# Kernel tuning notes

Measured on AMD Instinct MI355X. Metric: run time of the kernel, lower is better.

Reference implementation:

```python
import jax, jax.numpy as jnp
import numpy as np

N = 4608      # total nodes (48 graphs x 96 nodes)
B = 48
NPG = 96
D = 512       # vec_dim
XD = 16       # x_dim
E = N * 32    # GAT edges
L = 6         # GAT layers


def _w(k, shape, fan_in):
    return jax.random.normal(k, shape, jnp.float32) * (1.0 / np.sqrt(fan_in))


def setup_inputs() -> dict:
    key = jax.random.key(0)
    ks = jax.random.split(key, 24)
    x = jax.random.normal(ks[0], (N, XD), jnp.float32)
    xyz = jax.random.normal(ks[1], (N, 3), jnp.float32)
    edge_index = jax.random.randint(ks[2], (2, E), 0, N, dtype=jnp.int32)
    ptr = (jnp.arange(B + 1) * NPG).astype(jnp.int32)
    # complete graph with replacement per segment (torch.combinations order: i<=j)
    i, j = np.triu_indices(NPG)
    offs = (np.arange(B) * NPG)[:, None]
    cloud_edge_index = jnp.asarray(
        np.stack([(i[None, :] + offs).reshape(-1), (j[None, :] + offs).reshape(-1)]),
        jnp.int32)
    return {
        'x': x, 'edge_index': edge_index, 'ptr': ptr, 'xyz': xyz,
        'cloud_edge_index': cloud_edge_index,
        'x_proj_w': _w(ks[3], (XD, D), XD), 'x_proj_b': jnp.zeros((D,), jnp.float32),
        'gat_wl': _w(ks[4], (L, D, D), D), 'gat_bl': jnp.zeros((L, D), jnp.float32),
        'gat_wr': _w(ks[5], (L, D, D), D), 'gat_br': jnp.zeros((L, D), jnp.float32),
        'gat_att': _w(ks[6], (L, D), D), 'gat_bias': jnp.zeros((L, D), jnp.float32),
        'gat_ln_g': jnp.ones((L - 1, D), jnp.float32), 'gat_ln_b': jnp.zeros((L - 1, D), jnp.float32),
        'cg_xyz_w': _w(ks[7], (3, D), 3),
        'cg_bn_g': jnp.ones((D,), jnp.float32), 'cg_bn_b': jnp.zeros((D,), jnp.float32),
        'cg_lin1_w': _w(ks[8], (D, D), D), 'cg_lin1_b': jnp.zeros((D,), jnp.float32),
        'cg_ln_g': jnp.ones((D,), jnp.float32), 'cg_ln_b': jnp.zeros((D,), jnp.float32),
        'lin_w': _w(ks[9], (D, D), D), 'lin_b': jnp.zeros((D,), jnp.float32),
        'bn_g': jnp.ones((D,), jnp.float32), 'bn_b': jnp.zeros((D,), jnp.float32),
    }


def _batchnorm(t, g, b):
    mu = t.mean(0)
    v = ((t - mu) ** 2).mean(0)
    return (t - mu) / jnp.sqrt(v + 1e-5) * g + b


def _forward(x, edge_index, cloud_edge_index, x_proj_w, x_proj_b, gat_wl, gat_bl,
             gat_wr, gat_br, gat_att, gat_bias, gat_ln_g, gat_ln_b, cg_xyz_w,
             cg_bn_g, cg_bn_b, cg_lin1_w, cg_lin1_b, cg_ln_g, cg_ln_b,
             lin_w, lin_b, bn_g, bn_b, xyz):
    n = x.shape[0]
    h = x @ x_proj_w + x_proj_b  # [N, D]
    # ---- GATv2 stack (heads=1, self-loops added, eval mode: no dropout) ----
    loops = jnp.arange(n, dtype=edge_index.dtype)
    ei = jnp.concatenate([edge_index, jnp.stack([loops, loops])], axis=1)
    src, dst = ei[0], ei[1]
    xg = h
    for l in range(L):
        xl = xg @ gat_wl[l] + gat_bl[l]
        xr = xg @ gat_wr[l] + gat_br[l]
        e = jax.nn.leaky_relu(xl[src] + xr[dst], 0.2) @ gat_att[l]  # [E+N]
        m = jax.ops.segment_max(e, dst, num_segments=n)
        ew = jnp.exp(e - m[dst])
        den = jax.ops.segment_sum(ew, dst, num_segments=n)
        alpha = ew / den[dst]
        out = jax.ops.segment_sum(alpha[:, None] * xl[src], dst, num_segments=n) + gat_bias[l]
        if l < L - 1:
            # PyG LayerNorm, mode='graph', batch=None: normalize over all elements
            mu = out.mean()
            sd = jnp.sqrt(((out - mu) ** 2).mean())
            out = (out - mu) / (sd + 1e-5) * gat_ln_g[l] + gat_ln_b[l]
            out = jax.nn.relu(out)
        xg = out
    # ---- CloudGraph (complete graph gather-compute-scatter) ----
    a, b = cloud_edge_index[0], cloud_edge_index[1]
    rx = h[a] - h[b]          # [Ec, D]
    rz = xyz[a] - xyz[b]      # [Ec, 3]
    sq = (rz ** 2).sum(-1)
    dist = jnp.where(sq > 0, jnp.sqrt(jnp.where(sq > 0, sq, 1.0)), 0.0)
    w = jnp.exp(-dist)[:, None]
    p1 = jax.ops.segment_sum(jax.nn.relu((w * rx) @ cg_lin1_w + cg_lin1_b), a, num_segments=n)
    mu1 = p1.mean(-1, keepdims=True)
    v1 = ((p1 - mu1) ** 2).mean(-1, keepdims=True)
    ln1 = (p1 - mu1) / jnp.sqrt(v1 + 1e-5) * cg_ln_g + cg_ln_b
    p2 = jax.ops.segment_sum(jax.nn.relu(rz @ cg_xyz_w), a, num_segments=n)
    xc = h + ln1 + _batchnorm(p2, cg_bn_g, cg_bn_b)
    # ---- fuse + final norm ----
    return _batchnorm((h + xg + xc) @ lin_w + lin_b, bn_g, bn_b)


def reference(x, edge_index, ptr, xyz, cloud_edge_index, x_proj_w, x_proj_b,
              gat_wl, gat_bl, gat_wr, gat_br, gat_att, gat_bias, gat_ln_g,
              gat_ln_b, cg_xyz_w, cg_bn_g, cg_bn_b, cg_lin1_w, cg_lin1_b,
              cg_ln_g, cg_ln_b, lin_w, lin_b, bn_g, bn_b):
    return _forward(x, edge_index, cloud_edge_index, x_proj_w, x_proj_b, gat_wl,
                    gat_bl, gat_wr, gat_br, gat_att, gat_bias, gat_ln_g,
                    gat_ln_b, cg_xyz_w, cg_bn_g, cg_bn_b, cg_lin1_w, cg_lin1_b,
                    cg_ln_g, cg_ln_b, lin_w, lin_b, bn_g, bn_b, xyz)
```

## Files before the change

### kernel.cpp

```cpp
#include <hip/hip_runtime.h>
#include <hip/hip_bf16.h>

#define NN 4608
#define BG 48
#define NPG 96
#define DD 512
#define XDIM 16
#define EREAL 147456
#define NLAYER 6
#define NK 262144
#define TRIU 4656

typedef __hip_bfloat16 bf16;
typedef short short8 __attribute__((ext_vector_type(8)));
typedef float f32x4 __attribute__((ext_vector_type(4)));
typedef float f32x2 __attribute__((ext_vector_type(2)));

__device__ __forceinline__ float s2f(short s) {
  return __uint_as_float(((unsigned int)(unsigned short)s) << 16);
}
__device__ __forceinline__ short f2bs(float f) {
  bf16 h = __float2bfloat16(f);
  short s;
  __builtin_memcpy(&s, &h, 2);
  return s;
}
__device__ __forceinline__ unsigned char f2f8(float v) {
  return (unsigned char)(__builtin_amdgcn_cvt_pk_fp8_f32(v, v, 0, false) & 0xff);
}
__device__ __forceinline__ void f8x4(unsigned int w, float* o) {
  f32x2 a = __builtin_amdgcn_cvt_pk_f32_fp8(w, false);
  f32x2 b = __builtin_amdgcn_cvt_pk_f32_fp8(w, true);
  o[0] = a[0]; o[1] = a[1]; o[2] = b[0]; o[3] = b[1];
}

__global__ __launch_bounds__(256) void k_wt(const float* __restrict__ wl,
                                            const float* __restrict__ wr,
                                            const float* __restrict__ cg,
                                            const float* __restrict__ lin,
                                            bf16* __restrict__ Wt,
                                            int* __restrict__ counts,
                                            float* __restrict__ statsAll) {
  if (blockIdx.z == 0) {
    int id = (blockIdx.y * 16 + blockIdx.x) * 256 + threadIdx.x;
    if (id < NN) counts[id] = 0;
    if (id < 5 * 32) statsAll[id] = 0.f;
  }
  __shared__ float tile[32][33];
  int z = blockIdx.z;
  const float* src = (z < 6) ? wl + (size_t)z * NK
                   : (z < 12) ? wr + (size_t)(z - 6) * NK
                   : (z == 12) ? cg : lin;
  bf16* dst = Wt + (size_t)z * NK;
  int c = threadIdx.x & 31;
  int r0 = threadIdx.x >> 5;
  int bx = blockIdx.x * 32, by = blockIdx.y * 32;
#pragma unroll
  for (int i = 0; i < 4; i++) {
    int r = r0 + i * 8;
    tile[r][c] = src[(size_t)(by + r) * 512 + bx + c];
  }
  __syncthreads();
#pragma unroll
  for (int i = 0; i < 4; i++) {
    int r = r0 + i * 8;
    dst[(size_t)(bx + r) * 512 + by + c] = __float2bfloat16(tile[c][r]);
  }
}

__global__ void k_xproj(const float* __restrict__ x, const float* __restrict__ w,
                        const float* __restrict__ b, const int* __restrict__ ei,
                        const float* __restrict__ xyz,
                        bf16* __restrict__ h_bf, int* __restrict__ counts,
                        float* __restrict__ ep) {
  int i = blockIdx.x * blockDim.x + threadIdx.x;
  if (i >= NN * DD) return;
  if (i < EREAL) atomicAdd(&counts[ei[EREAL + i]], 1);
  if (i < NN * NPG) {
    int n = i / NPG, e = i - n * NPG;
    int p = n % NPG;
    if (e < NPG - p) {
      int g = n / NPG;
      int slot = g * TRIU + p * NPG - (p * (p - 1)) / 2 + e;
      int j = n + e;
      float dx = xyz[n * 3] - xyz[j * 3];
      float dy = xyz[n * 3 + 1] - xyz[j * 3 + 1];
      float dz = xyz[n * 3 + 2] - xyz[j * 3 + 2];
      float sq = dx * dx + dy * dy + dz * dz;
      float dist = (sq > 0.f) ? sqrtf(sq) : 0.f;
      float4 v;
      v.x = dx; v.y = dy; v.z = dz; v.w = __expf(-dist);
      *(float4*)&ep[(size_t)slot * 4] = v;
    }
  }
  int n = i >> 9, d = i & 511;
  float acc = b[d];
#pragma unroll
  for (int k = 0; k < XDIM; k++) acc += x[n * XDIM + k] * w[k * DD + d];
  h_bf[i] = __float2bfloat16(acc);
}

__global__ void k_scan(const int* __restrict__ counts, int* offsets, int* cursor) {
  __shared__ int part[256];
  __shared__ int pre[256];
  int t = threadIdx.x;
  int base = t * 18;
  int s = 0;
#pragma unroll
  for (int i = 0; i < 18; i++) s += counts[base + i];
  part[t] = s;
  __syncthreads();
  if (t == 0) {
    int r = 0;
    for (int i = 0; i < 256; i++) { pre[i] = r; r += part[i]; }
  }
  __syncthreads();
  int run = pre[t];
#pragma unroll
  for (int i = 0; i < 18; i++) {
    offsets[base + i] = run;
    cursor[base + i] = run;
    run += counts[base + i];
  }
  if (t == 0) offsets[NN] = EREAL;
}
__global__ void k_scatter(const int* __restrict__ ei, int* cursor, int* ssrc) {
  int e = blockIdx.x * blockDim.x + threadIdx.x;
  if (e < EREAL) {
    int s = ei[e], d = ei[EREAL + e];
    int pos = atomicAdd(&cursor[d], 1);
    ssrc[pos] = s;
  }
}

__global__ __launch_bounds__(256) void k_gemm(
    const bf16* __restrict__ Abf,
    const bf16* __restrict__ B0, const bf16* __restrict__ B1,
    const float* __restrict__ bias0, const float* __restrict__ bias1,
    float* __restrict__ C0, float* __restrict__ C1,
    bf16* __restrict__ Cb0, bf16* __restrict__ Cb1,
    unsigned char* __restrict__ Cf8_0, unsigned char* __restrict__ Cf8_1,
    const float* __restrict__ statsIn,
    const float* __restrict__ lng, const float* __restrict__ lnb,
    float* __restrict__ zptr, int zn,
    float* __restrict__ csum, float* __restrict__ csq) {
  if (zptr && blockIdx.x == 0 && blockIdx.y == 0 && blockIdx.z == 0) {
    for (int i = threadIdx.x; i < zn; i += 256) zptr[i] = 0.f;
  }
  __shared__ __align__(16) bf16 As[128 * 40];
  __shared__ __align__(16) bf16 Bs[64 * 40];
  __shared__ float cs[64], cq[64];
  const bf16* B = blockIdx.z ? B1 : B0;
  const float* bias = blockIdx.z ? bias1 : bias0;
  float* C = blockIdx.z ? C1 : C0;
  bf16* Cb = blockIdx.z ? Cb1 : Cb0;
  unsigned char* Cf8 = blockIdx.z ? Cf8_1 : Cf8_0;
  int tid = threadIdx.x;
  int m0 = blockIdx.x * 128, n0 = blockIdx.y * 64;
  int lane = tid & 63, wid = tid >> 6;
  int mh = (wid >> 1) * 64, nh = (wid & 1) * 32;
  int l15 = lane & 15, quad = lane >> 4;

  if (csum && tid < 64) { cs[tid] = 0.f; cq[tid] = 0.f; }

  float mu = 0.f, inv = 1.f;
  if (statsIn) {
    float s = 0.f, ss = 0.f;
#pragma unroll
    for (int i = 0; i < 16; i++) { s += statsIn[i]; ss += statsIn[16 + i]; }
    const float invM = 1.f / ((float)NN * (float)DD);
    mu = s * invM;
    float var = ss * invM - mu * mu;
    float sd = sqrtf(fmaxf(var, 0.f));
    inv = 1.f / (sd + 1e-5f);
  }

  f32x4 acc[4][2];
#pragma unroll
  for (int mt = 0; mt < 4; mt++)
#pragma unroll
    for (int nt = 0; nt < 2; nt++) acc[mt][nt] = (f32x4)0.f;

  for (int k0 = 0; k0 < 512; k0 += 32) {
    if (statsIn) {
#pragma unroll
      for (int it = 0; it < 2; it++) {
        int idx = tid + it * 256;
        int row = idx >> 2, kc = (idx & 3) * 8;
        short8 raw = *(const short8*)&Abf[(size_t)(m0 + row) * 512 + k0 + kc];
        float4 ga = *(const float4*)&lng[k0 + kc];
        float4 gb = *(const float4*)&lng[k0 + kc + 4];
        float4 ba = *(const float4*)&lnb[k0 + kc];
        float4 bb = *(const float4*)&lnb[k0 + kc + 4];
        float gg[8] = {ga.x, ga.y, ga.z, ga.w, gb.x, gb.y, gb.z, gb.w};
        float bv[8] = {ba.x, ba.y, ba.z, ba.w, bb.x, bb.y, bb.z, bb.w};
        short8 pk;
#pragma unroll
        for (int k = 0; k < 8; k++) {
          float t = fmaxf((s2f(raw[k]) - mu) * inv * gg[k] + bv[k], 0.f);
          pk[k] = f2bs(t);
        }
        *(short8*)&As[row * 40 + kc] = pk;
      }
    } else {
#pragma unroll
      for (int it = 0; it < 2; it++) {
        int idx = tid + it * 256;
        int row = idx >> 2, kc = (idx & 3) * 8;
        *(short8*)&As[row * 40 + kc] =
            *(const short8*)&Abf[(size_t)(m0 + row) * 512 + k0 + kc];
      }
    }
    {
      int row = tid >> 2, kc = (tid & 3) * 8;
      *(short8*)&Bs[row * 40 + kc] =
          *(const short8*)&B[(size_t)(n0 + row) * 512 + k0 + kc];
    }
    __syncthreads();
    short8 af[4], bfr[2];
#pragma unroll
    for (int mt = 0; mt < 4; mt++)
      af[mt] = *(const short8*)&As[(mh + mt * 16 + l15) * 40 + quad * 8];
#pragma unroll
    for (int nt = 0; nt < 2; nt++)
      bfr[nt] = *(const short8*)&Bs[(nh + nt * 16 + l15) * 40 + quad * 8];
#pragma unroll
    for (int mt = 0; mt < 4; mt++)
#pragma unroll
      for (int nt = 0; nt < 2; nt++)
        acc[mt][nt] = __builtin_amdgcn_mfma_f32_16x16x32_bf16(
            af[mt], bfr[nt], acc[mt][nt], 0, 0, 0);
    __syncthreads();
  }
  float colS[2] = {0.f, 0.f}, colQ[2] = {0.f, 0.f};
#pragma unroll
  for (int mt = 0; mt < 4; mt++) {
#pragma unroll
    for (int nt = 0; nt < 2; nt++) {
      int col = n0 + nh + nt * 16 + l15;
      float bv = bias ? bias[col] : 0.f;
#pragma unroll
      for (int r = 0; r < 4; r++) {
        int row = m0 + mh + mt * 16 + quad * 4 + r;
        float v = acc[mt][nt][r] + bv;
        if (C) C[(size_t)row * 512 + col] = v;
        if (Cb) Cb[(size_t)row * 512 + col] = __float2bfloat16(v);
        if (Cf8) Cf8[(size_t)row * 512 + col] = f2f8(v);
        if (csum) { colS[nt] += v; colQ[nt] += v * v; }
      }
    }
  }
  if (csum) {
#pragma unroll
    for (int nt = 0; nt < 2; nt++) {
      atomicAdd(&cs[nh + nt * 16 + l15], colS[nt]);
      atomicAdd(&cq[nh + nt * 16 + l15], colQ[nt]);
    }
    __syncthreads();
    if (tid < 64) {
      atomicAdd(&csum[n0 + tid], cs[tid]);
      atomicAdd(&csq[n0 + tid], cq[tid]);
    }
  }
}

__global__ __launch_bounds__(256) void k_gat_edge(const unsigned char* __restrict__ xl8,
                                                  const bf16* __restrict__ xr,
                                                  const float* __restrict__ att,
                                                  const float* __restrict__ bias,
                                                  const int* __restrict__ offs,
                                                  const int* __restrict__ ssrc,
                                                  bf16* __restrict__ out,
                                                  float* __restrict__ statsOut) {
  __shared__ float redS[4], redSS[4];
  int wave = (blockIdx.x * blockDim.x + threadIdx.x) >> 6;
  int lane = threadIdx.x & 63;
  int wid = threadIdx.x >> 6;
  if (wave < NN) {
    int n = wave;
    int base = lane * 8;
    float xrv[8], attv[8], acc[8];
    short8 xr8 = *(const short8*)&xr[(size_t)n * 512 + base];
#pragma unroll
    for (int k = 0; k < 8; k++) {
      xrv[k] = s2f(xr8[k]);
      attv[k] = att[base + k];
    }
    float m0, lsum;
    {
      uint2 q = *(const uint2*)&xl8[(size_t)n * 512 + base];
      float xs[8];
      f8x4(q.x, xs);
      f8x4(q.y, xs + 4);
      float sc0 = 0.f;
#pragma unroll
      for (int k = 0; k < 8; k++) {
        acc[k] = xs[k];
        float t = xs[k] + xrv[k];
        t = (t > 0.f) ? t : 0.2f * t;
        sc0 += attv[k] * t;
      }
#pragma unroll
      for (int off = 32; off >= 1; off >>= 1) sc0 += __shfl_xor(sc0, off, 64);
      m0 = sc0;
      lsum = 1.f;
    }
    int e0 = offs[n], e1 = offs[n + 1];
    int e = e0;
    for (; e + 3 < e1; e += 4) {
      int s0 = ssrc[e], s1 = ssrc[e + 1], s2 = ssrc[e + 2], s3 = ssrc[e + 3];
      uint2 q0 = *(const uint2*)&xl8[(size_t)s0 * 512 + base];
      uint2 q1 = *(const uint2*)&xl8[(size_t)s1 * 512 + base];
      uint2 q2 = *(const uint2*)&xl8[(size_t)s2 * 512 + base];
      uint2 q3 = *(const uint2*)&xl8[(size_t)s3 * 512 + base];
      float x0[8], x1[8], x2[8], x3[8];
      f8x4(q0.x, x0); f8x4(q0.y, x0 + 4);
      f8x4(q1.x, x1); f8x4(q1.y, x1 + 4);
      f8x4(q2.x, x2); f8x4(q2.y, x2 + 4);
      f8x4(q3.x, x3); f8x4(q3.y, x3 + 4);
      float c0 = 0.f, c1 = 0.f, c2 = 0.f, c3 = 0.f;
#pragma unroll
      for (int k = 0; k < 8; k++) {
        float t0 = x0[k] + xrv[k]; t0 = (t0 > 0.f) ? t0 : 0.2f * t0; c0 += attv[k] * t0;
        float t1 = x1[k] + xrv[k]; t1 = (t1 > 0.f) ? t1 : 0.2f * t1; c1 += attv[k] * t1;
        float t2 = x2[k] + xrv[k]; t2 = (t2 > 0.f) ? t2 : 0.2f * t2; c2 += attv[k] * t2;
        float t3 = x3[k] + xrv[k]; t3 = (t3 > 0.f) ? t3 : 0.2f * t3; c3 += attv[k] * t3;
      }
#pragma unroll
      for (int off = 32; off >= 1; off >>= 1) {
        c0 += __shfl_xor(c0, off, 64);
        c1 += __shfl_xor(c1, off, 64);
        c2 += __shfl_xor(c2, off, 64);
        c3 += __shfl_xor(c3, off, 64);
      }
      float p0 = __expf(c0 - m0), p1 = __expf(c1 - m0);
      float p2 = __expf(c2 - m0), p3 = __expf(c3 - m0);
      lsum += p0 + p1 + p2 + p3;
#pragma unroll
      for (int k = 0; k < 8; k++)
        acc[k] += p0 * x0[k] + p1 * x1[k] + p2 * x2[k] + p3 * x3[k];
    }
    for (; e < e1; ++e) {
      int s0 = ssrc[e];
      uint2 q = *(const uint2*)&xl8[(size_t)s0 * 512 + base];
      float x0[8];
      f8x4(q.x, x0);
      f8x4(q.y, x0 + 4);
      float sc0 = 0.f;
#pragma unroll
      for (int k = 0; k < 8; k++) {
        float t0 = x0[k] + xrv[k];
        t0 = (t0 > 0.f) ? t0 : 0.2f * t0;
        sc0 += attv[k] * t0;
      }
#pragma unroll
      for (int off = 32; off >= 1; off >>= 1) sc0 += __shfl_xor(sc0, off, 64);
      float p0 = __expf(sc0 - m0);
      lsum += p0;
#pragma unroll
      for (int k = 0; k < 8; k++) acc[k] += p0 * x0[k];
    }
    float inv = 1.f / lsum;
    float o[8];
    float s = 0.f, ss = 0.f;
    short8 o8;
#pragma unroll
    for (int k = 0; k < 8; k++) {
      o[k] = acc[k] * inv + bias[base + k];
      s += o[k];
      ss += o[k] * o[k];
      o8[k] = f2bs(o[k]);
    }
    *(short8*)&out[(size_t)n * 512 + base] = o8;
    if (statsOut) {
#pragma unroll
      for (int off = 32; off >= 1; off >>= 1) {
        s += __shfl_xor(s, off, 64);
        ss += __shfl_xor(ss, off, 64);
      }
      if (lane == 0) { redS[wid] = s; redSS[wid] = ss; }
    }
  }
  if (statsOut) {
    __syncthreads();
    if (threadIdx.x == 0) {
      float a = redS[0] + redS[1] + redS[2] + redS[3];
      float b = redSS[0] + redSS[1] + redSS[2] + redSS[3];
      int slot = blockIdx.x & 15;
      atomicAdd(&statsOut[slot], a);
      atomicAdd(&statsOut[16 + slot], b);
    }
  }
}

__global__ __launch_bounds__(256) void k_cloud(const bf16* __restrict__ g1,
                                               const float* __restrict__ ep,
                                               const float* __restrict__ lin1b,
                                               const float* __restrict__ w3,
                                               float* __restrict__ p1,
                                               float* __restrict__ p2) {
  int w = (blockIdx.x * blockDim.x + threadIdx.x) >> 6;
  int lane = threadIdx.x & 63;
  if (w >= NN * 2) return;
  int qf = w & 3;
  int pi = w >> 2;
  int g = pi / 48, pp = pi % 48;
  int d0 = qf * 128 + lane * 2;
  float bb0 = lin1b[d0], bb1 = lin1b[d0 + 1];
  float w00 = w3[d0], w01 = w3[d0 + 1];
  float w10 = w3[512 + d0], w11 = w3[512 + d0 + 1];
  float w20 = w3[1024 + d0], w21 = w3[1024 + d0 + 1];

#pragma unroll
  for (int half = 0; half < 2; half++) {
    int p = half ? (NPG - 1 - pp) : pp;
    int n = g * NPG + p;
    int cnt = NPG - p;
    int slot0 = g * TRIU + p * NPG - (p * (p - 1)) / 2;
    unsigned int giw = *(const unsigned int*)&g1[(size_t)n * 512 + d0];
    float gi0 = s2f((short)(giw & 0xffff));
    float gi1 = s2f((short)(giw >> 16));
    float a10 = 0.f, a11 = 0.f, a20 = 0.f, a21 = 0.f;
    int e = 0;
    for (; e + 1 < cnt; e += 2) {
      float4 pa = *(const float4*)&ep[(size_t)(slot0 + e) * 4];
      float4 pb = *(const float4*)&ep[(size_t)(slot0 + e + 1) * 4];
      unsigned int gaw = *(const unsigned int*)&g1[(size_t)(n + e) * 512 + d0];
      unsigned int gbw = *(const unsigned int*)&g1[(size_t)(n + e + 1) * 512 + d0];
      float t;
      t = fmaf(pa.w, gi0 - s2f((short)(gaw & 0xffff)), bb0); a10 += fmaxf(t, 0.f);
      t = fmaf(pa.w, gi1 - s2f((short)(gaw >> 16)), bb1);    a11 += fmaxf(t, 0.f);
      t = fmaf(pb.w, gi0 - s2f((short)(gbw & 0xffff)), bb0); a10 += fmaxf(t, 0.f);
      t = fmaf(pb.w, gi1 - s2f((short)(gbw >> 16)), bb1);    a11 += fmaxf(t, 0.f);
      t = pa.x * w00 + pa.y * w10 + pa.z * w20; a20 += fmaxf(t, 0.f);
      t = pa.x * w01 + pa.y * w11 + pa.z * w21; a21 += fmaxf(t, 0.f);
      t = pb.x * w00 + pb.y * w10 + pb.z * w20; a20 += fmaxf(t, 0.f);
      t = pb.x * w01 + pb.y * w11 + pb.z * w21; a21 += fmaxf(t, 0.f);
    }
    if (e < cnt) {
      float4 pa = *(const float4*)&ep[(size_t)(slot0 + e) * 4];
      unsigned int gaw = *(const unsigned int*)&g1[(size_t)(n + e) * 512 + d0];
      float t;
      t = fmaf(pa.w, gi0 - s2f((short)(gaw & 0xffff)), bb0); a10 += fmaxf(t, 0.f);
      t = fmaf(pa.w, gi1 - s2f((short)(gaw >> 16)), bb1);    a11 += fmaxf(t, 0.f);
      t = pa.x * w00 + pa.y * w10 + pa.z * w20; a20 += fmaxf(t, 0.f);
      t = pa.x * w01 + pa.y * w11 + pa.z * w21; a21 += fmaxf(t, 0.f);
    }
    float2 o1, o2;
    o1.x = a10; o1.y = a11;
    o2.x = a20; o2.y = a21;
    *(float2*)&p1[(size_t)n * 512 + d0] = o1;
    *(float2*)&p2[(size_t)n * 512 + d0] = o2;
  }
}

__global__ __launch_bounds__(256) void k_cloud_epi(
    const float* __restrict__ p1, const float* __restrict__ p2,
    const bf16* __restrict__ h_bf, const bf16* __restrict__ xg_bf,
    const float* __restrict__ colsum, const float* __restrict__ colsq,
    const float* __restrict__ lng, const float* __restrict__ lnb,
    const float* __restrict__ bng, const float* __restrict__ bnb,
    bf16* __restrict__ s_bf, float* __restrict__ zptr) {
  if (blockIdx.x == 0) {
    for (int i = threadIdx.x; i < 1024; i += 256) zptr[i] = 0.f;
  }
  int wave = (blockIdx.x * blockDim.x + threadIdx.x) >> 6;
  int lane = threadIdx.x & 63;
  if (wave >= NN) return;
  int n = wave;
  size_t rb = (size_t)n * 512 + lane * 8;
  int base = lane * 8;
  float v[8];
  float s = 0.f;
#pragma unroll
  for (int k = 0; k < 8; k++) {
    v[k] = p1[rb + k];
    s += v[k];
  }
#pragma unroll
  for (int off = 32; off >= 1; off >>= 1) s += __shfl_xor(s, off, 64);
  float mu = s * (1.f / 512.f);
  float ss = 0.f;
#pragma unroll
  for (int k = 0; k < 8; k++) {
    float t = v[k] - mu;
    ss += t * t;
  }
#pragma unroll
  for (int off = 32; off >= 1; off >>= 1) ss += __shfl_xor(ss, off, 64);
  float inv = 1.f / sqrtf(ss * (1.f / 512.f) + 1e-5f);
  short8 hb = *(const short8*)&h_bf[rb];
  short8 xb = *(const short8*)&xg_bf[rb];
  short8 o8;
#pragma unroll
  for (int k = 0; k < 8; k++) {
    int d = base + k;
    float ln1 = (v[k] - mu) * inv * lng[d] + lnb[d];
    float cmu = colsum[d] * (1.f / NN);
    float cvar = colsq[d] * (1.f / NN) - cmu * cmu;
    float cinv = 1.f / sqrtf(fmaxf(cvar, 0.f) + 1e-5f);
    float bnv = (p2[rb + k] - cmu) * cinv * bng[d] + bnb[d];
    float out = 2.f * s2f(hb[k]) + s2f(xb[k]) + ln1 + bnv;
    o8[k] = f2bs(out);
  }
  *(short8*)&s_bf[rb] = o8;
}

__global__ void k_col_reduce(const float* __restrict__ x, float* colsum, float* colsq) {
  int r0 = blockIdx.x * 128;
  int c0 = threadIdx.x;
  float s0 = 0.f, q0 = 0.f, s1 = 0.f, q1 = 0.f;
  for (int r = r0; r < r0 + 128; ++r) {
    float v = x[(size_t)r * 512 + c0];
    s0 += v;
    q0 += v * v;
    float w = x[(size_t)r * 512 + c0 + 256];
    s1 += w;
    q1 += w * w;
  }
  atomicAdd(&colsum[c0], s0);
  atomicAdd(&colsq[c0], q0);
  atomicAdd(&colsum[c0 + 256], s1);
  atomicAdd(&colsq[c0 + 256], q1);
}
__global__ void k_bn_out(const float* __restrict__ y, const float* __restrict__ colsum,
                         const float* __restrict__ colsq, const float* __restrict__ g,
                         const float* __restrict__ b, float* __restrict__ out) {
  int i = blockIdx.x * blockDim.x + threadIdx.x;
  if (i >= NN * DD) return;
  int d = i & 511;
  float mu = colsum[d] * (1.f / NN);
  float var = colsq[d] * (1.f / NN) - mu * mu;
  float inv = 1.f / sqrtf(fmaxf(var, 0.f) + 1e-5f);
  out[i] = (y[i] - mu) * inv * g[d] + b[d];
}

extern "C" void kernel_launch(void* const* d_in, const int* in_sizes, int n_in,
                              void* d_out, int out_size, void* d_ws, size_t ws_size,
                              hipStream_t stream) {
  const float* x = (const float*)d_in[0];
  const int* ei = (const int*)d_in[1];
  const float* xyz = (const float*)d_in[3];
  const float* x_proj_w = (const float*)d_in[5];
  const float* x_proj_b = (const float*)d_in[6];
  const float* gat_wl = (const float*)d_in[7];
  const float* gat_bl = (const float*)d_in[8];
  const float* gat_wr = (const float*)d_in[9];
  const float* gat_br = (const float*)d_in[10];
  const float* gat_att = (const float*)d_in[11];
  const float* gat_bias = (const float*)d_in[12];
  const float* gat_ln_g = (const float*)d_in[13];
  const float* gat_ln_b = (const float*)d_in[14];
  const float* cg_xyz_w = (const float*)d_in[15];
  const float* cg_bn_g = (const float*)d_in[16];
  const float* cg_bn_b = (const float*)d_in[17];
  const float* cg_lin1_w = (const float*)d_in[18];
  const float* cg_lin1_b = (const float*)d_in[19];
  const float* cg_ln_g = (const float*)d_in[20];
  const float* cg_ln_b = (const float*)d_in[21];
  const float* lin_w = (const float*)d_in[22];
  const float* lin_b = (const float*)d_in[23];
  const float* bn_g = (const float*)d_in[24];
  const float* bn_b = (const float*)d_in[25];

  const size_t ND = (size_t)NN * DD;
  char* w = (char*)d_ws;
  float* p1 = (float*)w;       w += ND * 4;
  float* p2 = (float*)w;       w += ND * 4;
  bf16* h_bf = (bf16*)w;       w += ND * 2;
  bf16* xg_bf = (bf16*)w;      w += ND * 2;
  bf16* g1_bf = (bf16*)w;      w += ND * 2;
  bf16* xr_bf = (bf16*)w;      w += ND * 2;
  unsigned char* xl_f8 = (unsigned char*)w; w += ND;
  bf16* Wt = (bf16*)w;         w += (size_t)14 * NK * 2;
  float* eparam = (float*)w;   w += (size_t)BG * TRIU * 16;
  int* counts = (int*)w;       w += NN * 4;
  int* offs = (int*)w;         w += (NN + 4) * 4;
  int* cursor = (int*)w;       w += NN * 4;
  int* ssrc = (int*)w;         w += EREAL * 4;
  float* statsAll = (float*)w; w += 5 * 32 * 4;
  float* colsum = (float*)w;   w += 512 * 4;
  float* colsq = (float*)w;    w += 512 * 4;
  float* colsum2 = (float*)w;  w += 512 * 4;
  float* colsq2 = (float*)w;   w += 512 * 4;
  float* y = p1;
  bf16* s_bf = h_bf;

  const int TPB = 256;
  const int ND_BLK = (int)((ND + TPB - 1) / TPB);

  k_wt<<<dim3(16, 16, 14), TPB, 0, stream>>>(gat_wl, gat_wr, cg_lin1_w, lin_w, Wt,
                                             counts, statsAll);
  k_xproj<<<ND_BLK, TPB, 0, stream>>>(x, x_proj_w, x_proj_b, ei, xyz, h_bf,
                                      counts, eparam);
  k_scan<<<1, 256, 0, stream>>>(counts, offs, cursor);
  k_scatter<<<(EREAL + TPB - 1) / TPB, TPB, 0, stream>>>(ei, cursor, ssrc);

  for (int l = 0; l < NLAYER; l++) {
    const bf16* A = (l == 0) ? h_bf : xg_bf;
    const float* sIn = (l > 0) ? statsAll + 32 * (l - 1) : nullptr;
    const float* lg = (l > 0) ? gat_ln_g + (l - 1) * DD : nullptr;
    const float* lb = (l > 0) ? gat_ln_b + (l - 1) * DD : nullptr;
    k_gemm<<<dim3(36, 8, 2), TPB, 0, stream>>>(
        A, Wt + (size_t)l * NK, Wt + (size_t)(6 + l) * NK,
        gat_bl + l * DD, gat_br + l * DD, nullptr, nullptr, nullptr, xr_bf,
        xl_f8, nullptr, sIn, lg, lb, nullptr, 0, nullptr, nullptr);
    float* sOut = (l < NLAYER - 1) ? statsAll + 32 * l : nullptr;
    k_gat_edge<<<NN / 4, TPB, 0, stream>>>(xl_f8, xr_bf, gat_att + l * DD,
                                           gat_bias + l * DD, offs, ssrc,
                                           xg_bf, sOut);
  }

  k_gemm<<<dim3(36, 8, 1), TPB, 0, stream>>>(
      h_bf, Wt + (size_t)12 * NK, Wt + (size_t)12 * NK, nullptr, nullptr,
      nullptr, nullptr, g1_bf, g1_bf, nullptr, nullptr, nullptr, nullptr, nullptr,
      colsum, 1024, nullptr, nullptr);
  k_cloud<<<NN / 2, TPB, 0, stream>>>(g1_bf, eparam, cg_lin1_b, cg_xyz_w, p1, p2);
  k_col_reduce<<<36, 256, 0, stream>>>(p2, colsum, colsq);
  k_cloud_epi<<<NN / 4, TPB, 0, stream>>>(p1, p2, h_bf, xg_bf, colsum, colsq,
                                          cg_ln_g, cg_ln_b, cg_bn_g, cg_bn_b,
                                          s_bf, colsum2);

  k_gemm<<<dim3(36, 8, 1), TPB, 0, stream>>>(
      s_bf, Wt + (size_t)13 * NK, Wt + (size_t)13 * NK, lin_b, lin_b,
      y, y, nullptr, nullptr, nullptr, nullptr, nullptr, nullptr, nullptr,
      nullptr, 0, colsum2, colsq2);
  k_bn_out<<<ND_BLK, TPB, 0, stream>>>(y, colsum2, colsq2, bn_g, bn_b,
                                       (float*)d_out);
}
```

Baseline: 591.0 us.

## Double-buffer GEMM tiles via global_load_lds and split LayerNorm into separate kernel

```diff
diff --git a/kernel.cpp b/kernel.cpp
--- a/kernel.cpp
+++ b/kernel.cpp
@@ -32,6 +32,12 @@
   f32x2 a = __builtin_amdgcn_cvt_pk_f32_fp8(w, false);
   f32x2 b = __builtin_amdgcn_cvt_pk_f32_fp8(w, true);
   o[0] = a[0]; o[1] = a[1]; o[2] = b[0]; o[3] = b[1];
+}
+
+typedef const __attribute__((address_space(1))) unsigned int ga_u32;
+typedef __attribute__((address_space(3))) unsigned int ls_u32;
+__device__ __forceinline__ void gl16(const void* g, void* l) {
+  __builtin_amdgcn_global_load_lds((ga_u32*)g, (ls_u32*)l, 16, 0, 0);
 }
 
 __global__ __launch_bounds__(256) void k_wt(const float* __restrict__ wl,
@@ -133,6 +139,32 @@
   }
 }
 
+__global__ __launch_bounds__(256) void k_ln(const bf16* __restrict__ in,
+                                            bf16* __restrict__ out,
+                                            const float* __restrict__ stats,
+                                            const float* __restrict__ g,
+                                            const float* __restrict__ b) {
+  float s = 0.f, ss = 0.f;
+#pragma unroll
+  for (int i = 0; i < 16; i++) { s += stats[i]; ss += stats[16 + i]; }
+  const float invM = 1.f / ((float)NN * (float)DD);
+  float mu = s * invM;
+  float var = ss * invM - mu * mu;
+  float sd = sqrtf(fmaxf(var, 0.f));
+  float inv = 1.f / (sd + 1e-5f);
+  int i = blockIdx.x * 256 + threadIdx.x;
+  int base = i * 8;
+  int d0 = base & 511;
+  short8 raw = *(const short8*)&in[base];
+  short8 pk;
+#pragma unroll
+  for (int k = 0; k < 8; k++) {
+    float t = fmaxf((s2f(raw[k]) - mu) * inv * g[d0 + k] + b[d0 + k], 0.f);
+    pk[k] = f2bs(t);
+  }
+  *(short8*)&out[base] = pk;
+}
+
 __global__ __launch_bounds__(256) void k_gemm(
     const bf16* __restrict__ Abf,
     const bf16* __restrict__ B0, const bf16* __restrict__ B1,
@@ -140,15 +172,13 @@
     float* __restrict__ C0, float* __restrict__ C1,
     bf16* __restrict__ Cb0, bf16* __restrict__ Cb1,
     unsigned char* __restrict__ Cf8_0, unsigned char* __restrict__ Cf8_1,
-    const float* __restrict__ statsIn,
-    const float* __restrict__ lng, const float* __restrict__ lnb,
     float* __restrict__ zptr, int zn,
     float* __restrict__ csum, float* __restrict__ csq) {
   if (zptr && blockIdx.x == 0 && blockIdx.y == 0 && blockIdx.z == 0) {
     for (int i = threadIdx.x; i < zn; i += 256) zptr[i] = 0.f;
   }
-  __shared__ __align__(16) bf16 As[128 * 40];
-  __shared__ __align__(16) bf16 Bs[64 * 40];
+  __shared__ __align__(16) bf16 As[2][128 * 32];
+  __shared__ __align__(16) bf16 Bs[2][64 * 32];
   __shared__ float cs[64], cq[64];
   const bf16* B = blockIdx.z ? B1 : B0;
   const float* bias = blockIdx.z ? bias1 : bias0;
@@ -160,20 +190,19 @@
   int lane = tid & 63, wid = tid >> 6;
   int mh = (wid >> 1) * 64, nh = (wid & 1) * 32;
   int l15 = lane & 15, quad = lane >> 4;
+  int lrow = lane >> 2, lkc = (lane & 3) * 8;
 
   if (csum && tid < 64) { cs[tid] = 0.f; cq[tid] = 0.f; }
 
-  float mu = 0.f, inv = 1.f;
-  if (statsIn) {
-    float s = 0.f, ss = 0.f;
-#pragma unroll
-    for (int i = 0; i < 16; i++) { s += statsIn[i]; ss += statsIn[16 + i]; }
-    const float invM = 1.f / ((float)NN * (float)DD);
-    mu = s * invM;
-    float var = ss * invM - mu * mu;
-    float sd = sqrtf(fmaxf(var, 0.f));
-    inv = 1.f / (sd + 1e-5f);
-  }
+  const bf16* aSrc0 = Abf + (size_t)(m0 + wid * 16 + lrow) * 512 + lkc;
+  const bf16* aSrc1 = Abf + (size_t)(m0 + 64 + wid * 16 + lrow) * 512 + lkc;
+  const bf16* bSrc  = B   + (size_t)(n0 + wid * 16 + lrow) * 512 + lkc;
+
+#define STAGE(bi, kk) do {                                  \
+    gl16(aSrc0 + (kk) * 32, &As[bi][wid * 512]);            \
+    gl16(aSrc1 + (kk) * 32, &As[bi][2048 + wid * 512]);     \
+    gl16(bSrc  + (kk) * 32, &Bs[bi][wid * 512]);            \
+  } while (0)
 
   f32x4 acc[4][2];
 #pragma unroll
@@ -181,49 +210,20 @@
 #pragma unroll
     for (int nt = 0; nt < 2; nt++) acc[mt][nt] = (f32x4)0.f;
 
-  for (int k0 = 0; k0 < 512; k0 += 32) {
-    if (statsIn) {
-#pragma unroll
-      for (int it = 0; it < 2; it++) {
-        int idx = tid + it * 256;
-        int row = idx >> 2, kc = (idx & 3) * 8;
-        short8 raw = *(const short8*)&Abf[(size_t)(m0 + row) * 512 + k0 + kc];
-        float4 ga = *(const float4*)&lng[k0 + kc];
-        float4 gb = *(const float4*)&lng[k0 + kc + 4];
-        float4 ba = *(const float4*)&lnb[k0 + kc];
-        float4 bb = *(const float4*)&lnb[k0 + kc + 4];
-        float gg[8] = {ga.x, ga.y, ga.z, ga.w, gb.x, gb.y, gb.z, gb.w};
-        float bv[8] = {ba.x, ba.y, ba.z, ba.w, bb.x, bb.y, bb.z, bb.w};
-        short8 pk;
-#pragma unroll
-        for (int k = 0; k < 8; k++) {
-          float t = fmaxf((s2f(raw[k]) - mu) * inv * gg[k] + bv[k], 0.f);
-          pk[k] = f2bs(t);
-        }
-        *(short8*)&As[row * 40 + kc] = pk;
-      }
-    } else {
-#pragma unroll
-      for (int it = 0; it < 2; it++) {
-        int idx = tid + it * 256;
-        int row = idx >> 2, kc = (idx & 3) * 8;
-        *(short8*)&As[row * 40 + kc] =
-            *(const short8*)&Abf[(size_t)(m0 + row) * 512 + k0 + kc];
-      }
-    }
-    {
-      int row = tid >> 2, kc = (tid & 3) * 8;
-      *(short8*)&Bs[row * 40 + kc] =
-          *(const short8*)&B[(size_t)(n0 + row) * 512 + k0 + kc];
-    }
-    __syncthreads();
+  STAGE(0, 0);
+  __syncthreads();
+
+#pragma unroll
+  for (int kt = 0; kt < 16; kt++) {
+    const int cur = kt & 1;
+    if (kt < 15) STAGE(cur ^ 1, kt + 1);
     short8 af[4], bfr[2];
 #pragma unroll
     for (int mt = 0; mt < 4; mt++)
-      af[mt] = *(const short8*)&As[(mh + mt * 16 + l15) * 40 + quad * 8];
+      af[mt] = *(const short8*)&As[cur][(mh + mt * 16 + l15) * 32 + quad * 8];
 #pragma unroll
     for (int nt = 0; nt < 2; nt++)
-      bfr[nt] = *(const short8*)&Bs[(nh + nt * 16 + l15) * 40 + quad * 8];
+      bfr[nt] = *(const short8*)&Bs[cur][(nh + nt * 16 + l15) * 32 + quad * 8];
 #pragma unroll
     for (int mt = 0; mt < 4; mt++)
 #pragma unroll
@@ -232,6 +232,8 @@
             af[mt], bfr[nt], acc[mt][nt], 0, 0, 0);
     __syncthreads();
   }
+#undef STAGE
+
   float colS[2] = {0.f, 0.f}, colQ[2] = {0.f, 0.f};
 #pragma unroll
   for (int mt = 0; mt < 4; mt++) {
@@ -585,6 +587,7 @@
   float* colsq2 = (float*)w;   w += 512 * 4;
   float* y = p1;
   bf16* s_bf = h_bf;
+  bf16* aln_bf = g1_bf;
 
   const int TPB = 256;
   const int ND_BLK = (int)((ND + TPB - 1) / TPB);
@@ -597,14 +600,19 @@
   k_scatter<<<(EREAL + TPB - 1) / TPB, TPB, 0, stream>>>(ei, cursor, ssrc);
 
   for (int l = 0; l < NLAYER; l++) {
-    const bf16* A = (l == 0) ? h_bf : xg_bf;
-    const float* sIn = (l > 0) ? statsAll + 32 * (l - 1) : nullptr;
-    const float* lg = (l > 0) ? gat_ln_g + (l - 1) * DD : nullptr;
-    const float* lb = (l > 0) ? gat_ln_b + (l - 1) * DD : nullptr;
+    const bf16* A;
+    if (l == 0) {
+      A = h_bf;
+    } else {
+      k_ln<<<(int)(ND / 8 / TPB), TPB, 0, stream>>>(
+          xg_bf, aln_bf, statsAll + 32 * (l - 1),
+          gat_ln_g + (size_t)(l - 1) * DD, gat_ln_b + (size_t)(l - 1) * DD);
+      A = aln_bf;
+    }
     k_gemm<<<dim3(36, 8, 2), TPB, 0, stream>>>(
         A, Wt + (size_t)l * NK, Wt + (size_t)(6 + l) * NK,
         gat_bl + l * DD, gat_br + l * DD, nullptr, nullptr, nullptr, xr_bf,
-        xl_f8, nullptr, sIn, lg, lb, nullptr, 0, nullptr, nullptr);
+        xl_f8, nullptr, nullptr, 0, nullptr, nullptr);
     float* sOut = (l < NLAYER - 1) ? statsAll + 32 * l : nullptr;
     k_gat_edge<<<NN / 4, TPB, 0, stream>>>(xl_f8, xr_bf, gat_att + l * DD,
                                            gat_bias + l * DD, offs, ssrc,
@@ -613,7 +621,7 @@
 
   k_gemm<<<dim3(36, 8, 1), TPB, 0, stream>>>(
       h_bf, Wt + (size_t)12 * NK, Wt + (size_t)12 * NK, nullptr, nullptr,
-      nullptr, nullptr, g1_bf, g1_bf, nullptr, nullptr, nullptr, nullptr, nullptr,
+      nullptr, nullptr, g1_bf, g1_bf, nullptr, nullptr,
       colsum, 1024, nullptr, nullptr);
   k_cloud<<<NN / 2, TPB, 0, stream>>>(g1_bf, eparam, cg_lin1_b, cg_xyz_w, p1, p2);
   k_col_reduce<<<36, 256, 0, stream>>>(p2, colsum, colsq);
@@ -623,7 +631,7 @@
 
   k_gemm<<<dim3(36, 8, 1), TPB, 0, stream>>>(
       s_bf, Wt + (size_t)13 * NK, Wt + (size_t)13 * NK, lin_b, lin_b,
-      y, y, nullptr, nullptr, nullptr, nullptr, nullptr, nullptr, nullptr,
+      y, y, nullptr, nullptr, nullptr, nullptr,
       nullptr, 0, colsum2, colsq2);
   k_bn_out<<<ND_BLK, TPB, 0, stream>>>(y, colsum2, colsq2, bn_g, bn_b,
                                        (float*)d_out);
```

Result: faster. 569.4 us (-3.7%).
